# Kernel tuning notes

Hardware: AMD Instinct MI355X
Metric: run time of the kernel (lower is better)

The kernel has to match this reference:

```python
import math
import jax, jax.numpy as jnp
import numpy as np

EMBED_DIM = 512
NUM_HEADS = 8
HEAD_DIM = EMBED_DIM // NUM_HEADS
NUM_EDGE_TYPES = 10
N = 2048  # nodes
B = 1


def setup_inputs() -> dict:
    key = jax.random.key(0)
    ks = jax.random.split(key, 8)
    s = 1.0 / math.sqrt(EMBED_DIM)
    return {
        "query": jax.random.normal(ks[0], (N, B, EMBED_DIM), jnp.float32),
        "key": jax.random.normal(ks[1], (N, B, EMBED_DIM), jnp.float32),
        "value": jax.random.normal(ks[2], (N, B, EMBED_DIM), jnp.float32),
        "edge_id_mat": jax.random.randint(ks[3], (N, N), 0, NUM_EDGE_TYPES, jnp.int32),
        "in_proj_weight": jax.random.normal(ks[4], (3 * EMBED_DIM, EMBED_DIM), jnp.float32) * s,
        "in_proj_bias": jnp.zeros((3 * EMBED_DIM,), jnp.float32),
        "out_proj_weight": jax.random.normal(ks[5], (EMBED_DIM, EMBED_DIM), jnp.float32) * s,
        "out_proj_bias": jnp.zeros((EMBED_DIM,), jnp.float32),
        "edge_embs_K": jax.random.normal(ks[6], (NUM_EDGE_TYPES, HEAD_DIM), jnp.float32),
    }


def reference(query, key, value, edge_id_mat, in_proj_weight, in_proj_bias,
              out_proj_weight, out_proj_bias, edge_embs_K):
    L, Bsz, E = query.shape
    H, hd = NUM_HEADS, HEAD_DIM
    w_q, w_k, w_v = jnp.split(in_proj_weight, 3, axis=0)
    b_q, b_k, b_v = jnp.split(in_proj_bias, 3)
    q = query @ w_q.T + b_q   # (L, B, E)
    k = key @ w_k.T + b_k
    v = value @ w_v.T + b_v

    def split_heads(x):
        # (L, B, E) -> (B*H, L, hd)  (matches torch view(L, B*H, hd).transpose(0,1))
        return x.reshape(L, Bsz * H, hd).transpose(1, 0, 2)

    q = split_heads(q) / math.sqrt(hd)  # torch scales by sqrt(E=head_dim)
    k = split_heads(k)
    v = split_heads(v)

    attn = jnp.einsum('bnd,bmd->bnm', q, k)  # (B*H, L, L)

    # edge-type score bias: edge_attn[b,i,j] = q[b,i,:] . edge_embs_K[edge_id_mat[i,j], :]
    # computed efficiently as per-type scores then a gather (avoids (L,L,hd) tensor)
    type_scores = jnp.einsum('bnd,td->bnt', q, edge_embs_K)  # (B*H, L, T)
    idx = jnp.broadcast_to(edge_id_mat[None, :, :], attn.shape)
    edge_attn = jnp.take_along_axis(type_scores, idx, axis=2)  # (B*H, L, L)
    attn = jax.nn.softmax(attn + edge_attn, axis=-1)

    out = jnp.einsum('bnm,bmd->bnd', attn, v)           # (B*H, L, hd)
    out = out.transpose(1, 0, 2).reshape(L, Bsz, E)      # (L, B, E)
    out = out @ out_proj_weight.T + out_proj_bias
    return out
```

## Files before the change

### kernel.cpp

```cpp
#include <hip/hip_runtime.h>
#include <hip/hip_bf16.h>

#define NHEAD 8
#define SEQ   2048
#define HD    64
#define EMB   512
#define NTYPE 10
#define JSPLIT 4

#define QKV_NT (3 * EMB / 64)
#define QKV_MT (SEQ / 64)
#define QKV_BLOCKS (QKV_NT * QKV_MT)
#define PACK_BLOCKS (SEQ * SEQ / 4 / 256)

#define QSCALE 0.180336878f

typedef unsigned short u16;
typedef __attribute__((ext_vector_type(8))) short short8;
typedef __attribute__((ext_vector_type(4))) float float4v;

union F8 { short8 v; uint4 u4; u16 us[8]; };

__device__ __forceinline__ float bf2f(u16 u){
  union { unsigned u; float f; } w; w.u = ((unsigned)u) << 16; return w.f;
}
__device__ __forceinline__ u16 f2bf(float f){
  union { float f; unsigned u; } w; w.f = f;
  unsigned u = w.u;
  u += 0x7fffu + ((u >> 16) & 1u);
  return (u16)(u >> 16);
}
__device__ __forceinline__ unsigned cvtpk(float lo, float hi){
  union { __hip_bfloat162 b; unsigned u; } w;
  w.b = __float22bfloat162_rn(float2{lo, hi});
  return w.u;
}
__device__ __forceinline__ uint4 pk8(float4 a, float4 b){
  uint4 p; p.x = cvtpk(a.x, a.y); p.y = cvtpk(a.z, a.w);
           p.z = cvtpk(b.x, b.y); p.w = cvtpk(b.z, b.w);
  return p;
}

__global__ __launch_bounds__(256) void fused_prep_gemm(
    const float* __restrict__ q, const float* __restrict__ k, const float* __restrict__ v,
    const float* __restrict__ ipw, const float* __restrict__ ipb, const int* __restrict__ eid,
    u16* __restrict__ Qs, u16* __restrict__ Kb, u16* __restrict__ Vb,
    unsigned* __restrict__ eidp)
{
  const int b = blockIdx.x;
  const int t = threadIdx.x;

  if (b >= QKV_BLOCKS) {
    const int i = (b - QKV_BLOCKS) * 256 + t;
    int4 vv = ((const int4*)eid)[i];
    eidp[i] = (unsigned)(vv.x & 0xff) | ((unsigned)(vv.y & 0xff) << 8) |
              ((unsigned)(vv.z & 0xff) << 16) | ((unsigned)(vv.w & 0xff) << 24);
    return;
  }

  __shared__ u16 As[64][72];
  __shared__ u16 Bs[64][72];

  const int X = b & 7, jb = b >> 3;
  const int mt = X * 4 + (jb & 3), nt = jb >> 2;
  const int n0 = nt * 64, m0 = mt * 64;
  const int z = n0 >> 9;
  const float* A = (z == 0) ? q : (z == 1) ? k : v;
  const float scale = (z == 0) ? QSCALE : 1.0f;

  const int w = t >> 6, lane = t & 63, lr = lane & 15, lg = lane >> 4;
  const int wm = w >> 1, wn = w & 1;
  const int srow = t >> 2, kb16 = (t & 3) * 16;

  float4v acc[2][2];
#pragma unroll
  for (int mi = 0; mi < 2; mi++)
#pragma unroll
    for (int ni = 0; ni < 2; ni++) acc[mi][ni] = (float4v){0.f, 0.f, 0.f, 0.f};

  const float* pa = A   + (size_t)(m0 + srow) * EMB + kb16;
  const float* pw = ipw + (size_t)(n0 + srow) * EMB + kb16;

  float4 a[4], bb[4];
#pragma unroll
  for (int j = 0; j < 4; j++) { a[j] = *(const float4*)(pa + j * 4); bb[j] = *(const float4*)(pw + j * 4); }

  for (int k0 = 0; k0 < EMB; k0 += 64) {
    *(uint4*)&As[srow][kb16]     = pk8(a[0], a[1]);
    *(uint4*)&As[srow][kb16 + 8] = pk8(a[2], a[3]);
    *(uint4*)&Bs[srow][kb16]     = pk8(bb[0], bb[1]);
    *(uint4*)&Bs[srow][kb16 + 8] = pk8(bb[2], bb[3]);
    __syncthreads();
    if (k0 + 64 < EMB) {
#pragma unroll
      for (int j = 0; j < 4; j++) {
        a[j]  = *(const float4*)(pa + k0 + 64 + j * 4);
        bb[j] = *(const float4*)(pw + k0 + 64 + j * 4);
      }
    }
    F8 af[2][2], bf_[2][2];
#pragma unroll
    for (int kc = 0; kc < 2; kc++) {
#pragma unroll
      for (int mi = 0; mi < 2; mi++)
        af[mi][kc].u4 = *(const uint4*)&As[wm * 32 + mi * 16 + lr][kc * 32 + lg * 8];
#pragma unroll
      for (int ni = 0; ni < 2; ni++)
        bf_[ni][kc].u4 = *(const uint4*)&Bs[wn * 32 + ni * 16 + lr][kc * 32 + lg * 8];
    }
#pragma unroll
    for (int kc = 0; kc < 2; kc++)
#pragma unroll
      for (int mi = 0; mi < 2; mi++)
#pragma unroll
        for (int ni = 0; ni < 2; ni++)
          acc[mi][ni] = __builtin_amdgcn_mfma_f32_16x16x32_bf16(af[mi][kc].v, bf_[ni][kc].v, acc[mi][ni], 0, 0, 0);
    __syncthreads();
  }

  u16* O = (z == 0) ? Qs : ((z == 1) ? Kb : Vb);
#pragma unroll
  for (int mi = 0; mi < 2; mi++) {
#pragma unroll
    for (int ni = 0; ni < 2; ni++) {
      const int n = n0 + wn * 32 + ni * 16 + lr;
      const int e = n & 511, h = e >> 6, d = e & 63;
      const float bias = ipb[n];
      const int mb = m0 + wm * 32 + mi * 16 + lg * 4;
      if (z < 2) {
#pragma unroll
        for (int r = 0; r < 4; r++)
          O[((size_t)h * SEQ + mb + r) * HD + d] = f2bf((acc[mi][ni][r] + bias) * scale);
      } else {
        ushort4 pk;
        pk.x = f2bf(acc[mi][ni][0] + bias); pk.y = f2bf(acc[mi][ni][1] + bias);
        pk.z = f2bf(acc[mi][ni][2] + bias); pk.w = f2bf(acc[mi][ni][3] + bias);
        *(ushort4*)(O + ((size_t)(h * HD + d)) * SEQ + mb) = pk;
      }
    }
  }
}

__global__ __launch_bounds__(256) void attn_kernel(
    const u16* __restrict__ Qs, const u16* __restrict__ Kb, const u16* __restrict__ Vb,
    const unsigned* __restrict__ eid32, const float* __restrict__ EK,
    u16* __restrict__ Upart, float* __restrict__ mpart, float* __restrict__ lpart)
{
  __shared__ u16 Kt[64][72];
  __shared__ u16 Vt[64][72];
  __shared__ u16 Pl[4][16][72];
  __shared__ float tsl[64][13];
  __shared__ float ekl[NTYPE][64];

  const int t = threadIdx.x;
  const int wave = t >> 6, lane = t & 63, lr = lane & 15, lg = lane >> 4;
  const int bb_ = blockIdx.x;
  const int X = bb_ & 7, jj = bb_ >> 3;
  const int p = X * 4 + (jj >> 5);
  const int i0 = (jj & 31) * 64;
  const int h  = p >> 2;
  const int z  = p & 3;

  for (int i = t; i < NTYPE * 64; i += 256) ekl[i >> 6][i & 63] = EK[i];
  __syncthreads();

  {
    const int row = t >> 2, tt = t & 3;
    const u16* qr = Qs + ((size_t)h * SEQ + i0 + row) * HD;
    float a0 = 0.f, a1 = 0.f, a2 = 0.f;
    for (int d0 = 0; d0 < HD; d0 += 8) {
      uint4 qq = *(const uint4*)(qr + d0);
      const u16* qu = (const u16*)&qq;
#pragma unroll
      for (int e = 0; e < 8; e++) {
        float qf = bf2f(qu[e]);
        a0 += qf * ekl[tt][d0 + e];
        a1 += qf * ekl[tt + 4][d0 + e];
        a2 += qf * ekl[(tt < 2) ? (tt + 8) : 8][d0 + e];
      }
    }
    tsl[row][tt] = a0; tsl[row][tt + 4] = a1;
    if (tt < 2) tsl[row][tt + 8] = a2;
  }

  F8 qf[2];
#pragma unroll
  for (int kc = 0; kc < 2; kc++)
    qf[kc].u4 = *(const uint4*)(Qs + ((size_t)h * SEQ + i0 + wave * 16 + lr) * HD + kc * 32 + lg * 8);

  float4v ao[4];
#pragma unroll
  for (int d = 0; d < 4; d++) ao[d] = (float4v){0.f, 0.f, 0.f, 0.f};
  float m_i = -1e30f, l_i = 0.f;

  const int srow = t >> 2, sdc = (t & 3) * 16;
  const int jbase = z * (SEQ / JSPLIT);
  const int NT = (SEQ / JSPLIT) / 64;
  const unsigned* erow = eid32 + (size_t)(i0 + wave * 16 + lr) * (SEQ / 4);

  uint4 kp0, kp1, vp0, vp1;
  unsigned ed[4], edn[4];
  {
    const u16* kp = Kb + ((size_t)h * SEQ + jbase + srow) * HD + sdc;
    kp0 = *(const uint4*)kp; kp1 = *(const uint4*)(kp + 8);
    const u16* vp = Vb + ((size_t)(h * HD + srow)) * SEQ + jbase + sdc;
    vp0 = *(const uint4*)vp; vp1 = *(const uint4*)(vp + 8);
    *(uint4*)&Kt[srow][sdc] = kp0; *(uint4*)&Kt[srow][sdc + 8] = kp1;
    *(uint4*)&Vt[srow][sdc] = vp0; *(uint4*)&Vt[srow][sdc + 8] = vp1;
    const int ej = jbase >> 2;
#pragma unroll
    for (int c = 0; c < 4; c++) ed[c] = erow[ej + c * 4 + lg];
  }

  for (int jt = 0; jt < NT; jt++) {
    __syncthreads();

    if (jt + 1 < NT) {
      const int jn = jbase + (jt + 1) * 64;
      const u16* kp = Kb + ((size_t)h * SEQ + jn + srow) * HD + sdc;
      kp0 = *(const uint4*)kp; kp1 = *(const uint4*)(kp + 8);
      const u16* vp = Vb + ((size_t)(h * HD + srow)) * SEQ + jn + sdc;
      vp0 = *(const uint4*)vp; vp1 = *(const uint4*)(vp + 8);
      const int ejn = jn >> 2;
#pragma unroll
      for (int c = 0; c < 4; c++) edn[c] = erow[ejn + c * 4 + lg];
    }

    float4v sacc[4];
#pragma unroll
    for (int c = 0; c < 4; c++) sacc[c] = (float4v){0.f, 0.f, 0.f, 0.f};
#pragma unroll
    for (int kc = 0; kc < 2; kc++) {
#pragma unroll
      for (int c = 0; c < 4; c++) {
        F8 kf; kf.u4 = *(const uint4*)&Kt[c * 16 + lr][kc * 32 + lg * 8];
        sacc[c] = __builtin_amdgcn_mfma_f32_16x16x32_bf16(kf.v, qf[kc].v, sacc[c], 0, 0, 0);
      }
    }

    float rmax = -1e30f;
#pragma unroll
    for (int c = 0; c < 4; c++) {
      const unsigned e = ed[c];
#pragma unroll
      for (int r = 0; r < 4; r++) {
        const float s = sacc[c][r] + tsl[wave * 16 + lr][(e >> (r * 8)) & 0xffu];
        sacc[c][r] = s;
        rmax = fmaxf(rmax, s);
      }
    }
    rmax = fmaxf(rmax, __shfl_xor(rmax, 16));
    rmax = fmaxf(rmax, __shfl_xor(rmax, 32));
    const float mnew = fmaxf(m_i, rmax);
    const float fct = exp2f(m_i - mnew);
    float rsum = 0.f;
#pragma unroll
    for (int c = 0; c < 4; c++) {
#pragma unroll
      for (int r = 0; r < 4; r++) {
        const float p_ = exp2f(sacc[c][r] - mnew);
        sacc[c][r] = p_;
        rsum += p_;
      }
    }
    rsum += __shfl_xor(rsum, 16);
    rsum += __shfl_xor(rsum, 32);
    l_i = l_i * fct + rsum;
    m_i = mnew;

#pragma unroll
    for (int c = 0; c < 4; c++) {
      uint2 pw;
      pw.x = cvtpk(sacc[c][0], sacc[c][1]);
      pw.y = cvtpk(sacc[c][2], sacc[c][3]);
      *(uint2*)&Pl[wave][lr][c * 16 + lg * 4] = pw;
    }
#pragma unroll
    for (int db = 0; db < 4; db++) {
#pragma unroll
      for (int r = 0; r < 4; r++) ao[db][r] *= fct;
    }
#pragma unroll
    for (int kc = 0; kc < 2; kc++) {
      F8 pf; pf.u4 = *(const uint4*)&Pl[wave][lr][kc * 32 + lg * 8];
#pragma unroll
      for (int db = 0; db < 4; db++) {
        F8 vf; vf.u4 = *(const uint4*)&Vt[db * 16 + lr][kc * 32 + lg * 8];
        ao[db] = __builtin_amdgcn_mfma_f32_16x16x32_bf16(vf.v, pf.v, ao[db], 0, 0, 0);
      }
    }

    __syncthreads();
    if (jt + 1 < NT) {
      *(uint4*)&Kt[srow][sdc] = kp0; *(uint4*)&Kt[srow][sdc + 8] = kp1;
      *(uint4*)&Vt[srow][sdc] = vp0; *(uint4*)&Vt[srow][sdc + 8] = vp1;
#pragma unroll
      for (int c = 0; c < 4; c++) ed[c] = edn[c];
    }
  }

  {
    const size_t base = (((size_t)z * NHEAD + h) * SEQ + i0) * HD;
    const int n = wave * 16 + lr;
#pragma unroll
    for (int db = 0; db < 4; db++) {
      uint2 pw;
      pw.x = cvtpk(ao[db][0], ao[db][1]);
      pw.y = cvtpk(ao[db][2], ao[db][3]);
      *(uint2*)(Upart + base + (size_t)n * HD + db * 16 + lg * 4) = pw;
    }
    if (lg == 0) {
      mpart[((size_t)z * NHEAD + h) * SEQ + i0 + n] = m_i;
      lpart[((size_t)z * NHEAD + h) * SEQ + i0 + n] = l_i;
    }
  }
}

__global__ __launch_bounds__(256) void combine_outproj(
    const u16* __restrict__ Upart, const float* __restrict__ mpart,
    const float* __restrict__ lpart, const float* __restrict__ opw,
    const float* __restrict__ opb, float* __restrict__ out)
{
  __shared__ u16 As[32][72];
  __shared__ u16 Bs[64][72];
  __shared__ float cww[JSPLIT][NHEAD][32];

  const int t = threadIdx.x;
  const int b = blockIdx.x;
  const int X = b & 7, jb = b >> 3;
  const int mt = X * 8 + (jb >> 3), nt = jb & 7;
  const int m0 = mt * 32, n0 = nt * 64;

  {
    const int hh = t >> 5, nl = t & 31;
    const int gn = m0 + nl;
    float mz[JSPLIT], wz[JSPLIT];
    float M = -1e30f;
#pragma unroll
    for (int zz = 0; zz < JSPLIT; zz++) {
      mz[zz] = mpart[((size_t)zz * NHEAD + hh) * SEQ + gn];
      M = fmaxf(M, mz[zz]);
    }
    float Ls = 0.f;
#pragma unroll
    for (int zz = 0; zz < JSPLIT; zz++) {
      wz[zz] = exp2f(mz[zz] - M);
      Ls += wz[zz] * lpart[((size_t)zz * NHEAD + hh) * SEQ + gn];
    }
    const float inv = 1.0f / Ls;
#pragma unroll
    for (int zz = 0; zz < JSPLIT; zz++) cww[zz][hh][nl] = wz[zz] * inv;
  }
  __syncthreads();

  const int w = t >> 6, lane = t & 63, lr = lane & 15, lg = lane >> 4;
  const int arow = t >> 3, akb = (t & 7) * 8;
  const int brow = t >> 2, bkb = (t & 3) * 16;

  float4v acc[2];
#pragma unroll
  for (int mi = 0; mi < 2; mi++) acc[mi] = (float4v){0.f, 0.f, 0.f, 0.f};

  const float* pw = opw + (size_t)(n0 + brow) * EMB + bkb;

  int hcur = akb >> 6, dcur = akb & 63;
  uint4 ua[JSPLIT];
#pragma unroll
  for (int zz = 0; zz < JSPLIT; zz++)
    ua[zz] = *(const uint4*)(Upart + (((size_t)zz * NHEAD + hcur) * SEQ + m0 + arow) * HD + dcur);
  float4 bbv[4];
#pragma unroll
  for (int j = 0; j < 4; j++) bbv[j] = *(const float4*)(pw + j * 4);

  for (int k0 = 0; k0 < EMB; k0 += 64) {
    {
      float cc[8];
#pragma unroll
      for (int j = 0; j < 8; j++) cc[j] = 0.f;
#pragma unroll
      for (int zz = 0; zz < JSPLIT; zz++) {
        const float wgt = cww[zz][hcur][arow];
        F8 q0; q0.u4 = ua[zz];
#pragma unroll
        for (int j = 0; j < 8; j++) cc[j] += wgt * bf2f((u16)q0.us[j]);
      }
      float4 c0 = {cc[0], cc[1], cc[2], cc[3]}, c1 = {cc[4], cc[5], cc[6], cc[7]};
      *(uint4*)&As[arow][akb] = pk8(c0, c1);
      *(uint4*)&Bs[brow][bkb]     = pk8(bbv[0], bbv[1]);
      *(uint4*)&Bs[brow][bkb + 8] = pk8(bbv[2], bbv[3]);
    }
    __syncthreads();
    if (k0 + 64 < EMB) {
      const int e = k0 + 64 + akb;
      hcur = e >> 6; dcur = e & 63;
#pragma unroll
      for (int zz = 0; zz < JSPLIT; zz++)
        ua[zz] = *(const uint4*)(Upart + (((size_t)zz * NHEAD + hcur) * SEQ + m0 + arow) * HD + dcur);
#pragma unroll
      for (int j = 0; j < 4; j++) bbv[j] = *(const float4*)(pw + k0 + 64 + j * 4);
    }
    F8 af[2][2], bf_[2];
#pragma unroll
    for (int kc = 0; kc < 2; kc++) {
#pragma unroll
      for (int mi = 0; mi < 2; mi++)
        af[mi][kc].u4 = *(const uint4*)&As[mi * 16 + lr][kc * 32 + lg * 8];
      bf_[kc].u4 = *(const uint4*)&Bs[w * 16 + lr][kc * 32 + lg * 8];
    }
#pragma unroll
    for (int kc = 0; kc < 2; kc++)
#pragma unroll
      for (int mi = 0; mi < 2; mi++)
        acc[mi] = __builtin_amdgcn_mfma_f32_16x16x32_bf16(af[mi][kc].v, bf_[kc].v, acc[mi], 0, 0, 0);
    __syncthreads();
  }

  const int n = n0 + w * 16 + lr;
  const float bias = opb[n];
#pragma unroll
  for (int mi = 0; mi < 2; mi++) {
    const int mb = m0 + mi * 16 + lg * 4;
#pragma unroll
    for (int r = 0; r < 4; r++)
      out[(size_t)(mb + r) * EMB + n] = acc[mi][r] + bias;
  }
}

extern "C" void kernel_launch(void* const* d_in, const int* in_sizes, int n_in,
                              void* d_out, int out_size, void* d_ws, size_t ws_size,
                              hipStream_t stream)
{
  const float* query = (const float*)d_in[0];
  const float* key_  = (const float*)d_in[1];
  const float* value = (const float*)d_in[2];
  const int*   eid   = (const int*)d_in[3];
  const float* ipw   = (const float*)d_in[4];
  const float* ipb   = (const float*)d_in[5];
  const float* opw   = (const float*)d_in[6];
  const float* opb   = (const float*)d_in[7];
  const float* ek    = (const float*)d_in[8];
  float* out = (float*)d_out;

  char* ws = (char*)d_ws;
  u16* Qs = (u16*)ws;              ws += (size_t)NHEAD * SEQ * HD * 2;
  u16* Kb = (u16*)ws;              ws += (size_t)NHEAD * SEQ * HD * 2;
  u16* Vb = (u16*)ws;              ws += (size_t)NHEAD * SEQ * HD * 2;
  unsigned* eidp = (unsigned*)ws;  ws += (size_t)SEQ * SEQ;
  u16* Upart = (u16*)ws;           ws += (size_t)JSPLIT * NHEAD * SEQ * HD * 2;
  float* mpart = (float*)ws;       ws += (size_t)JSPLIT * NHEAD * SEQ * 4;
  float* lpart = (float*)ws;       ws += (size_t)JSPLIT * NHEAD * SEQ * 4;

  fused_prep_gemm<<<dim3(QKV_BLOCKS + PACK_BLOCKS), dim3(256), 0, stream>>>(
      query, key_, value, ipw, ipb, eid, Qs, Kb, Vb, eidp);
  attn_kernel<<<dim3(SEQ / 64 * NHEAD * JSPLIT), dim3(256), 0, stream>>>(
      Qs, Kb, Vb, eidp, ek, Upart, mpart, lpart);
  combine_outproj<<<dim3((SEQ / 32) * (EMB / 64)), dim3(256), 0, stream>>>(
      Upart, mpart, lpart, opw, opb, out);
}
```

Before: 150.0 us.

## Feed P to PV MFMA from registers and double the key-split count

The PV product now uses a 16x16x16 bf16 MFMA that takes the softmax probabilities straight from registers, so the per-wave LDS staging buffer for P and its round trip are gone. The output accumulator layout flips, so the rescale factors are broadcast with shuffles and the partial outputs are written element by element. Separately, the key-dimension split goes from 4 to 8, doubling the attention grid for more parallelism but adding more partial results for the combine kernel to merge. The narrower MFMA issues twice as many instructions, and the scalar bf16 stores are less coalesced.

```diff
diff --git a/kernel.cpp b/kernel.cpp
--- a/kernel.cpp
+++ b/kernel.cpp
@@ -6,7 +6,7 @@
 #define HD    64
 #define EMB   512
 #define NTYPE 10
-#define JSPLIT 4
+#define JSPLIT 8
 
 #define QKV_NT (3 * EMB / 64)
 #define QKV_MT (SEQ / 64)
@@ -17,9 +17,11 @@
 
 typedef unsigned short u16;
 typedef __attribute__((ext_vector_type(8))) short short8;
+typedef __attribute__((ext_vector_type(4))) short short4v;
 typedef __attribute__((ext_vector_type(4))) float float4v;
 
 union F8 { short8 v; uint4 u4; u16 us[8]; };
+union PB { uint2 u2; short4v s4; };
 
 __device__ __forceinline__ float bf2f(u16 u){
   union { unsigned u; float f; } w; w.u = ((unsigned)u) << 16; return w.f;
@@ -39,6 +41,17 @@
   uint4 p; p.x = cvtpk(a.x, a.y); p.y = cvtpk(a.z, a.w);
            p.z = cvtpk(b.x, b.y); p.w = cvtpk(b.z, b.w);
   return p;
+}
+
+__device__ __forceinline__ void pv_mfma(float4v& ao, uint2 pa, uint2 vb){
+#if __has_builtin(__builtin_amdgcn_mfma_f32_16x16x16bf16_1k)
+  PB a; a.u2 = pa;
+  PB b; b.u2 = vb;
+  ao = __builtin_amdgcn_mfma_f32_16x16x16bf16_1k(a.s4, b.s4, ao, 0, 0, 0);
+#else
+  asm volatile("s_nop 1\n\tv_mfma_f32_16x16x16_bf16 %0, %1, %2, %0"
+               : "+v"(ao) : "v"(pa), "v"(vb));
+#endif
 }
 
 __global__ __launch_bounds__(256) void fused_prep_gemm(
@@ -148,7 +161,6 @@
 {
   __shared__ u16 Kt[64][72];
   __shared__ u16 Vt[64][72];
-  __shared__ u16 Pl[4][16][72];
   __shared__ float tsl[64][13];
   __shared__ float ekl[NTYPE][64];
 
@@ -156,10 +168,10 @@
   const int wave = t >> 6, lane = t & 63, lr = lane & 15, lg = lane >> 4;
   const int bb_ = blockIdx.x;
   const int X = bb_ & 7, jj = bb_ >> 3;
-  const int p = X * 4 + (jj >> 5);
+  const int p = X * 8 + (jj >> 5);
   const int i0 = (jj & 31) * 64;
-  const int h  = p >> 2;
-  const int z  = p & 3;
+  const int h  = p >> 3;
+  const int z  = p & 7;
 
   for (int i = t; i < NTYPE * 64; i += 256) ekl[i >> 6][i & 63] = EK[i];
   __syncthreads();
@@ -268,25 +280,26 @@
     l_i = l_i * fct + rsum;
     m_i = mnew;
 
+    uint2 pa_[4];
 #pragma unroll
     for (int c = 0; c < 4; c++) {
-      uint2 pw;
-      pw.x = cvtpk(sacc[c][0], sacc[c][1]);
-      pw.y = cvtpk(sacc[c][2], sacc[c][3]);
-      *(uint2*)&Pl[wave][lr][c * 16 + lg * 4] = pw;
-    }
+      pa_[c].x = cvtpk(sacc[c][0], sacc[c][1]);
+      pa_[c].y = cvtpk(sacc[c][2], sacc[c][3]);
+    }
+    float fctv[4];
+#pragma unroll
+    for (int rr = 0; rr < 4; rr++) fctv[rr] = __shfl(fct, lg * 4 + rr);
 #pragma unroll
     for (int db = 0; db < 4; db++) {
 #pragma unroll
-      for (int r = 0; r < 4; r++) ao[db][r] *= fct;
-    }
-#pragma unroll
-    for (int kc = 0; kc < 2; kc++) {
-      F8 pf; pf.u4 = *(const uint4*)&Pl[wave][lr][kc * 32 + lg * 8];
+      for (int rr = 0; rr < 4; rr++) ao[db][rr] *= fctv[rr];
+    }
+#pragma unroll
+    for (int c = 0; c < 4; c++) {
 #pragma unroll
       for (int db = 0; db < 4; db++) {
-        F8 vf; vf.u4 = *(const uint4*)&Vt[db * 16 + lr][kc * 32 + lg * 8];
-        ao[db] = __builtin_amdgcn_mfma_f32_16x16x32_bf16(vf.v, pf.v, ao[db], 0, 0, 0);
+        uint2 vb = *(const uint2*)&Vt[db * 16 + lr][c * 16 + lg * 4];
+        pv_mfma(ao[db], pa_[c], vb);
       }
     }
 
@@ -301,17 +314,17 @@
 
   {
     const size_t base = (((size_t)z * NHEAD + h) * SEQ + i0) * HD;
-    const int n = wave * 16 + lr;
 #pragma unroll
     for (int db = 0; db < 4; db++) {
-      uint2 pw;
-      pw.x = cvtpk(ao[db][0], ao[db][1]);
-      pw.y = cvtpk(ao[db][2], ao[db][3]);
-      *(uint2*)(Upart + base + (size_t)n * HD + db * 16 + lg * 4) = pw;
+#pragma unroll
+      for (int rr = 0; rr < 4; rr++) {
+        const int n = wave * 16 + lg * 4 + rr;
+        Upart[base + (size_t)n * HD + db * 16 + lr] = f2bf(ao[db][rr]);
+      }
     }
     if (lg == 0) {
-      mpart[((size_t)z * NHEAD + h) * SEQ + i0 + n] = m_i;
-      lpart[((size_t)z * NHEAD + h) * SEQ + i0 + n] = l_i;
+      mpart[((size_t)z * NHEAD + h) * SEQ + i0 + wave * 16 + lr] = m_i;
+      lpart[((size_t)z * NHEAD + h) * SEQ + i0 + wave * 16 + lr] = l_i;
     }
   }
 }
```

Result: slower. 153.5 us (+2.4%).
